# Kernel optimization log

Hardware: AMD Instinct MI355X
Metric: run time of the kernel (lower is better)

Reference implementation:

```python
import jax, jax.numpy as jnp
import numpy as np

# FrictionConfig constants (chosen in init_kwargs)
K_STEPS = 4
ETA = 0.1
ETA_DECAY = 0.9
MU_MAX = 10.0
SMOOTH_LAMBDA = 0.1
RADIUS = 8
B, S, H = 4, 2048, 1024
INNER = max(H // 2, 32)  # 512


def _build_window_edges(length, radius):
    chunks = []
    for d in range(1, radius + 1):
        i = np.arange(length - d, dtype=np.int32)
        chunks.append(np.stack([i, i + d], axis=1))
    return np.concatenate(chunks, axis=0)  # [E, 2]


def setup_inputs() -> dict:
    key = jax.random.key(0)
    ks = jax.random.split(key, 8)
    hidden = jax.random.normal(ks[0], (B, S, H), dtype=jnp.float32)
    attention_mask = jnp.ones((B, S), dtype=jnp.int32)
    edges = jnp.asarray(_build_window_edges(S, RADIUS))
    # edge_mlp: Linear(2, INNER) -> GELU -> Linear(INNER, 1)
    W1 = jax.random.normal(ks[1], (2, INNER), dtype=jnp.float32) * (1.0 / np.sqrt(2))
    b1 = jnp.zeros((INNER,), dtype=jnp.float32)
    W2 = jax.random.normal(ks[2], (INNER, 1), dtype=jnp.float32) * (1.0 / np.sqrt(INNER))
    b2 = jnp.zeros((1,), dtype=jnp.float32)
    # q_proj: Linear(H, H)
    Wq = jax.random.normal(ks[3], (H, H), dtype=jnp.float32) * (1.0 / np.sqrt(H))
    bq = jnp.zeros((H,), dtype=jnp.float32)
    # LayerNorm
    gamma = jnp.ones((H,), dtype=jnp.float32)
    beta = jnp.zeros((H,), dtype=jnp.float32)
    return {"hidden": hidden, "attention_mask": attention_mask, "edges": edges,
            "Wq": Wq, "bq": bq, "W1": W1, "b1": b1, "W2": W2, "b2": b2,
            "gamma": gamma, "beta": beta}


def _edge_weights(h, ei, ej, W1, b1, W2, b2):
    hi = h[ei]  # [E, H]
    hj = h[ej]
    diff = hi - hj
    dist = jnp.linalg.norm(diff, axis=-1, keepdims=True)           # [E, 1]
    ni = jnp.maximum(jnp.linalg.norm(hi, axis=-1), 1e-6)
    nj = jnp.maximum(jnp.linalg.norm(hj, axis=-1), 1e-6)
    cos = (jnp.sum(hi * hj, axis=-1) / (ni * nj))[:, None]         # [E, 1]
    feats = jnp.concatenate([dist, cos], axis=-1)                  # [E, 2]
    z = jax.nn.gelu(feats @ W1 + b1, approximate=False) @ W2 + b2  # [E, 1]
    return jax.nn.softplus(z) + 1e-5


def _laplacian(h, ei, ej, mu):
    n = h.shape[0]
    weighted = mu * (h[ei] - h[ej])  # [E, H]
    # normalize_laplacian = True
    w = mu[:, 0]
    deg = jnp.zeros((n,), h.dtype).at[ei].add(w).at[ej].add(w)
    inv_sqrt = jnp.maximum(deg, 1e-6) ** -0.5
    weighted = weighted * (inv_sqrt[ei] * inv_sqrt[ej])[:, None]
    lap = jnp.zeros_like(h).at[ei].add(weighted).at[ej].add(-weighted)
    return lap


def _smooth(s):
    left = jnp.concatenate([s[:1], s[:-1]], axis=0)
    right = jnp.concatenate([s[1:], s[-1:]], axis=0)
    return s - SMOOTH_LAMBDA * (2.0 * s - left - right)


def _layernorm(x, gamma, beta):
    m = x.mean(axis=-1, keepdims=True)
    v = x.var(axis=-1, keepdims=True)
    return (x - m) * jax.lax.rsqrt(v + 1e-5) * gamma + beta


def _run_single(h, ei, ej, Wq, bq, W1, b1, W2, b2, gamma, beta):
    q = h @ Wq + bq
    state = h
    mu = None
    for step in range(K_STEPS):
        mu = _edge_weights(state, ei, ej, W1, b1, W2, b2)  # recompute_mu=True
        mu = jnp.minimum(mu, MU_MAX)
        lap = _laplacian(state, ei, ej, mu)
        eta = ETA * (ETA_DECAY ** step)
        state = state - eta * (lap - q)
        state = _smooth(state)
    out = _layernorm(state + h, gamma, beta)
    diffs = state[ei] - state[ej]
    energy = 0.5 * jnp.sum(mu[:, 0] * jnp.sum(diffs * diffs, axis=-1))
    return out, energy


def reference(hidden, attention_mask, edges, Wq, bq, W1, b1, W2, b2, gamma, beta):
    # All masks are full-length, so edges are identical across batch and
    # the outer Python batch loop vectorizes to a vmap.
    ei, ej = edges[:, 0], edges[:, 1]
    outputs, energy = jax.vmap(
        lambda h: _run_single(h, ei, ej, Wq, bq, W1, b1, W2, b2, gamma, beta)
    )(hidden)
    return outputs, energy
```

## Files before the change

### kernel.cpp

```cpp
#include <hip/hip_runtime.h>

#define BB 4
#define SS 2048
#define HH 1024
#define TQ 32
#define TU 32
#define CW 256

typedef unsigned short u16;
typedef __bf16 bf16x8 __attribute__((ext_vector_type(8)));
typedef float f32x4 __attribute__((ext_vector_type(4)));

__device__ __forceinline__ float b2f(u16 u){
  union { unsigned int i; float f; } v; v.i = ((unsigned int)u) << 16; return v.f;
}
__device__ __forceinline__ u16 f2b(float f){
  union { float f; unsigned int i; } v; v.f = f;
  unsigned int x = v.i;
  return (u16)((x + 0x7fffu + ((x >> 16) & 1u)) >> 16);
}
__device__ __forceinline__ float4 u4f(ushort4 v){
  float4 o; o.x = b2f(v.x); o.y = b2f(v.y); o.z = b2f(v.z); o.w = b2f(v.w); return o;
}
__device__ __forceinline__ ushort4 f4u(float4 v){
  ushort4 o; o.x = f2b(v.x); o.y = f2b(v.y); o.z = f2b(v.z); o.w = f2b(v.w); return o;
}
__device__ __forceinline__ float wave_sum(float v){
  #pragma unroll
  for(int m = 32; m > 0; m >>= 1) v += __shfl_xor(v, m);
  return v;
}
__device__ __forceinline__ float pread(const void* p, int i, int f){
  return f ? b2f(((const u16*)p)[i]) : ((const float*)p)[i];
}
__device__ __forceinline__ int dflag(const void* gm){
  return (((const u16*)gm)[0] == 0x3F80u) ? 1 : 0;
}
__device__ __forceinline__ void gload16(const void* g, void* l){
  __builtin_amdgcn_global_load_lds((const __attribute__((address_space(1))) unsigned int*)g,
                                   (__attribute__((address_space(3))) unsigned int*)l, 16, 0, 0);
}
__device__ __forceinline__ float  g_load(const float* p){
  return __hip_atomic_load(p, __ATOMIC_RELAXED, __HIP_MEMORY_SCOPE_AGENT);
}
__device__ __forceinline__ float  part_add(float* p, float v){
  return __hip_atomic_fetch_add(p, v, __ATOMIC_RELAXED, __HIP_MEMORY_SCOPE_AGENT);
}
__device__ __forceinline__ int    cnt_add(int* p){
  return __hip_atomic_fetch_add(p, 1, __ATOMIC_RELAXED, __HIP_MEMORY_SCOPE_AGENT);
}

__global__ __launch_bounds__(256) void k_setup(const void* hidden, u16* __restrict__ s,
                                               const void* Wq, u16* __restrict__ Wt,
                                               const void* bq, const void* W1, const void* b1,
                                               const void* W2, const void* b2, const void* gm,
                                               const void* bt,
                                               float* bqc, float* b2c, float* gmc, float* btc,
                                               float4* mlp4s, float* mkeys,
                                               float* partials, int* ecnt){
  __shared__ u16 t[32][33];
  __shared__ float ka[512], kb[512], kc[512], kw[512], kk[512];
  int f = dflag(gm);
  int bid = blockIdx.x, tid = threadIdx.x;
  if(bid < 8192){
    size_t i4 = (size_t)bid*256 + tid;
    if(f){
      ((ushort4*)s)[i4] = ((const ushort4*)hidden)[i4];
    } else {
      ((ushort4*)s)[i4] = f4u(((const float4*)hidden)[i4]);
    }
  } else if(bid < 8192 + 1024){
    int bi = bid - 8192;
    int bx = bi & 31, by = bi >> 5;
    int tx = tid & 31, ty = tid >> 5;
    #pragma unroll
    for(int r = 0; r < 32; r += 8){
      int idx = (by*32 + ty + r)*HH + bx*32 + tx;
      float v = f ? b2f(((const u16*)Wq)[idx]) : ((const float*)Wq)[idx];
      t[ty + r][tx] = f2b(v);
    }
    __syncthreads();
    #pragma unroll
    for(int r = 0; r < 32; r += 8)
      Wt[(size_t)(bx*32 + ty + r)*HH + by*32 + tx] = t[tx][ty + r];
  } else {
    for(int i = tid; i < 1024; i += 256) bqc[i] = pread(bq, i, f);
    if(tid == 0) b2c[0] = pread(b2, 0, f);
    for(int i = tid; i < 1024; i += 256) gmc[i] = pread(gm, i, f);
    for(int i = tid; i < 1024; i += 256) btc[i] = pread(bt, i, f);
    if(tid < BB) partials[tid] = 0.f;
    if(tid == 0) ecnt[0] = 0;
    const float is2 = 0.70710678118654752f;
    for(int j = tid; j < 512; j += 256){
      float a = pread(W1, j, f)       * is2;
      float b = pread(W1, 512 + j, f) * is2;
      float c = pread(b1, j, f)       * is2;
      float w = pread(W2, j, f)       * is2;
      ka[j] = a; kb[j] = b; kc[j] = c; kw[j] = w;
      float aa = fabsf(a);
      kk[j] = (aa > 0.f) ? (4.f + fabsf(b) + fabsf(c)) * __builtin_amdgcn_rcpf(aa) : 3e38f;
    }
    __syncthreads();
    for(int j = tid; j < 512; j += 256){
      float kj = kk[j];
      int r = 0;
      for(int k = 0; k < 512; k++)
        r += (kk[k] < kj) || (kk[k] == kj && k < j);
      mlp4s[r] = make_float4(ka[j], kb[j], kc[j], kw[j]);
      mkeys[r] = kj;
    }
  }
}

__global__ __launch_bounds__(256) void k_qgemm(const u16* __restrict__ A, const u16* __restrict__ Wt,
                                               const float* __restrict__ bqc, u16* __restrict__ q){
  __shared__ u16 lA[128*32];
  __shared__ u16 lB[128*32];
  int m0 = blockIdx.x*128, n0 = blockIdx.y*128;
  int tid  = threadIdx.x;
  int wave = tid >> 6, lane = tid & 63;
  int wm = (wave >> 1)*64, wn = (wave & 1)*64;
  int quad = lane >> 4, l16 = lane & 15;
  int srow = tid >> 2;
  int scol = (tid & 3)*8;

  f32x4 acc[4][4];
  #pragma unroll
  for(int i = 0; i < 4; i++)
    #pragma unroll
    for(int j = 0; j < 4; j++) acc[i][j] = (f32x4){0.f,0.f,0.f,0.f};

  for(int k0 = 0; k0 < HH; k0 += 32){
    __syncthreads();
    gload16(A  + (size_t)(m0 + srow     )*HH + k0 + scol, &lA[ srow     *32 + scol]);
    gload16(A  + (size_t)(m0 + srow + 64)*HH + k0 + scol, &lA[(srow+64) *32 + scol]);
    gload16(Wt + (size_t)(n0 + srow     )*HH + k0 + scol, &lB[ srow     *32 + scol]);
    gload16(Wt + (size_t)(n0 + srow + 64)*HH + k0 + scol, &lB[(srow+64) *32 + scol]);
    __syncthreads();
    bf16x8 af[4];
    #pragma unroll
    for(int mt = 0; mt < 4; mt++)
      af[mt] = *(const bf16x8*)&lA[(wm + mt*16 + l16)*32 + quad*8];
    #pragma unroll
    for(int nt = 0; nt < 4; nt++){
      bf16x8 bf = *(const bf16x8*)&lB[(wn + nt*16 + l16)*32 + quad*8];
      #pragma unroll
      for(int mt = 0; mt < 4; mt++)
        acc[mt][nt] = __builtin_amdgcn_mfma_f32_16x16x32_bf16(af[mt], bf, acc[mt][nt], 0, 0, 0);
    }
  }
  #pragma unroll
  for(int nt = 0; nt < 4; nt++){
    int col = n0 + wn + nt*16 + l16;
    float bqv = bqc[col];
    #pragma unroll
    for(int mt = 0; mt < 4; mt++){
      #pragma unroll
      for(int r = 0; r < 4; r++){
        int row = m0 + wm + mt*16 + quad*4 + r;
        q[(size_t)row*HH + col] = f2b(acc[mt][nt][r] + bqv);
      }
    }
  }
}

__device__ __forceinline__ void gram_band8(const u16* __restrict__ s, int b, int i0,
                                           float* __restrict__ Gband, int tid){
  int wave = tid >> 6, lane = tid & 63;
  if(wave < 4){
    int ti = wave >> 1;
    int tj = (wave + 1) >> 1;
    int quad = lane >> 4, l16 = lane & 15;
    int ra = i0 + ti*16 + l16; if(ra > SS-1) ra = SS-1;
    int rb = i0 + tj*16 + l16; if(rb > SS-1) rb = SS-1;
    const u16* ar = s + ((size_t)b*SS + ra)*HH + quad*8;
    const u16* br = s + ((size_t)b*SS + rb)*HH + quad*8;
    f32x4 acc = (f32x4){0.f,0.f,0.f,0.f};
    #pragma unroll 8
    for(int k0 = 0; k0 < HH; k0 += 32){
      bf16x8 af = *(const bf16x8*)(ar + k0);
      bf16x8 bf = *(const bf16x8*)(br + k0);
      acc = __builtin_amdgcn_mfma_f32_16x16x32_bf16(af, bf, acc, 0, 0, 0);
    }
    #pragma unroll
    for(int r = 0; r < 4; r++){
      int gr = ti*16 + quad*4 + r;
      int dd = tj*16 + l16 - gr;
      if(dd >= 0 && dd <= 8) Gband[gr*9 + dd] = acc[r];
    }
  } else {
    for(int rr = wave - 4; rr < 8; rr += 4){
      int r = 32 + rr;
      int row = i0 + r; if(row > SS-1) row = SS-1;
      const ushort4* rp = (const ushort4*)(s + ((size_t)b*SS + row)*HH);
      float a = 0.f;
      #pragma unroll
      for(int c = 0; c < 4; c++){
        float4 v = u4f(rp[lane + 64*c]);
        a += v.x*v.x + v.y*v.y + v.z*v.z + v.w*v.w;
      }
      a = wave_sum(a);
      if(lane == 0) Gband[r*9] = a;
    }
  }
}

__global__ __launch_bounds__(512) void k_mu(const u16* __restrict__ s,
                                            const float4* __restrict__ mlp4s,
                                            const float* __restrict__ mkeys,
                                            const float* __restrict__ b2c,
                                            float* __restrict__ mu){
  __shared__ float Gband[40*9];
  __shared__ float4 wpk[512];
  __shared__ float skey[512];
  int b = blockIdx.y, i0 = blockIdx.x*TQ;
  int tid = threadIdx.x;
  wpk[tid] = mlp4s[tid]; skey[tid] = mkeys[tid];
  gram_band8(s, b, i0, Gband, tid);
  __syncthreads();

  int e = tid >> 1, h = tid & 1;
  int d = (e >> 5) + 1, k = e & 31;
  bool valid = (i0 + k + d) < SS;
  float gii = Gband[k*9], gjj = Gband[(k+d)*9], gij = Gband[k*9 + d];
  float dist = sqrtf(fmaxf(gii + gjj - 2.f*gij, 0.f));
  float ni = fmaxf(sqrtf(gii), 1e-6f);
  float nj = fmaxf(sqrtf(gjj), 1e-6f);
  float cosv = gij * __builtin_amdgcn_rcpf(ni * nj);
  if(!valid){ dist = 3e38f; cosv = 0.f; }

  float wmin = dist;
  #pragma unroll
  for(int m = 32; m > 0; m >>= 1) wmin = fminf(wmin, __shfl_xor(wmin, m));
  int lo = 0, hi = 512;
  while(lo < hi){ int mid = (lo + hi) >> 1; if(skey[mid] <= wmin) lo = mid + 1; else hi = mid; }
  int cut = lo - h*256; cut = (cut < 0) ? 0 : (cut > 256 ? 256 : cut);

  const float4* wp = &wpk[h*256];
  float acc = 0.f;
  int j = 0;
  #pragma unroll 4
  for(; j < cut; j++){
    float4 wv = wp[j];
    float x = fmaf(dist, wv.x, fmaf(cosv, wv.y, wv.z));
    acc = fmaf(x + fabsf(x), wv.w, acc);
  }
  #pragma unroll 2
  for(; j < 256; j++){
    float4 wv = wp[j];
    float x  = fmaf(dist, wv.x, fmaf(cosv, wv.y, wv.z));
    float ax = fabsf(x);
    float tt = __builtin_amdgcn_rcpf(fmaf(0.3275911f, ax, 1.f));
    float poly = ((((1.061405429f*tt - 1.453152027f)*tt + 1.421413741f)*tt
                   - 0.284496736f)*tt + 0.254829592f)*tt;
    float ape = ax * poly * __expf(-ax*ax);
    acc = fmaf(x + ax - ape, wv.w, acc);
  }
  acc += __shfl_xor(acc, 1);
  if(h == 0 && valid){
    float z  = acc + b2c[0];
    float sp = fmaxf(z, 0.f) + __logf(1.f + __expf(-fabsf(z)));
    mu[((size_t)b*8 + (d-1))*SS + (i0 + k)] = fminf(sp + 1e-5f, 10.0f);
  }
}

__global__ __launch_bounds__(256, 4) void k_upsm(const u16* __restrict__ sIn, u16* __restrict__ sOut,
                                                 const u16* __restrict__ q, const float* __restrict__ mu,
                                                 float eta){
  __shared__ u16 st[50*CW];
  __shared__ float invsS[50];
  __shared__ float muS[58*8];
  int i0 = blockIdx.x*TU, c0 = blockIdx.y*CW, b = blockIdx.z;
  int tid = threadIdx.x;

  for(int idx = tid; idx < 50*(CW/8); idx += 256){
    int r = idx >> 5, cc = idx & 31;
    int i = i0 - 9 + r;
    uint4 v = {0,0,0,0};
    if(i >= 0 && i < SS) v = *(const uint4*)(sIn + ((size_t)b*SS + i)*HH + c0 + cc*8);
    ((uint4*)st)[idx] = v;
  }
  for(int idx = tid; idx < 58*8; idx += 256){
    int ir = idx >> 3, d = (idx & 7) + 1;
    int i = i0 - 17 + ir;
    float v = 0.f;
    if(i >= 0 && i + d < SS) v = mu[((size_t)b*8 + d-1)*SS + i];
    muS[idx] = v;
  }
  __syncthreads();
  if(tid < 50){
    int ir = tid + 8;
    float deg = 0.f;
    #pragma unroll
    for(int d = 1; d <= 8; d++){
      deg += muS[ir*8 + d-1];
      deg += muS[(ir-d)*8 + d-1];
    }
    invsS[tid] = 1.0f / sqrtf(fmaxf(deg, 1e-6f));
  }
  __syncthreads();

  int rq = tid >> 6, lane = tid & 63;
  float4 ua = {0,0,0,0}, ub = {0,0,0,0}, uc = {0,0,0,0};
  #pragma unroll
  for(int k = 0; k < 10; k++){
    int ur = rq*8 + k;
    int i  = i0 - 1 + ur;
    float4 o = {0.f,0.f,0.f,0.f};
    if(i >= 0 && i < SS){
      int sr = ur + 8, vr = ur + 8, mr = ur + 16;
      float inv_i = invsS[vr];
      float4 si = u4f(((const ushort4*)(st + (size_t)sr*CW))[lane]);
      float A = 0.f;
      float4 acc = {0.f,0.f,0.f,0.f};
      #pragma unroll
      for(int d = 1; d <= 8; d++){
        float cR = muS[mr*8 + d-1]     * inv_i        * invsS[vr+d];
        float cL = muS[(mr-d)*8 + d-1] * invsS[vr-d]  * inv_i;
        A += cR + cL;
        float4 vR = u4f(((const ushort4*)(st + (size_t)(sr+d)*CW))[lane]);
        float4 vL = u4f(((const ushort4*)(st + (size_t)(sr-d)*CW))[lane]);
        acc.x -= cR*vR.x + cL*vL.x; acc.y -= cR*vR.y + cL*vL.y;
        acc.z -= cR*vR.z + cL*vL.z; acc.w -= cR*vR.w + cL*vL.w;
      }
      acc.x += A*si.x; acc.y += A*si.y; acc.z += A*si.z; acc.w += A*si.w;
      float4 qv = u4f(*(const ushort4*)(q + ((size_t)b*SS + i)*HH + c0 + lane*4));
      o.x = si.x - eta*(acc.x - qv.x);
      o.y = si.y - eta*(acc.y - qv.y);
      o.z = si.z - eta*(acc.z - qv.z);
      o.w = si.w - eta*(acc.w - qv.w);
    }
    ua = ub; ub = uc; uc = o;
    if(k >= 2){
      int rr = rq*8 + k - 2;
      int iout = i0 + rr;
      float4 cc2 = ub;
      float4 l  = (iout > 0)     ? ua : cc2;
      float4 r4 = (iout < SS-1)  ? uc : cc2;
      float4 oo;
      oo.x = cc2.x - 0.1f*(2.f*cc2.x - l.x - r4.x);
      oo.y = cc2.y - 0.1f*(2.f*cc2.y - l.y - r4.y);
      oo.z = cc2.z - 0.1f*(2.f*cc2.z - l.z - r4.z);
      oo.w = cc2.w - 0.1f*(2.f*cc2.w - l.w - r4.w);
      *(ushort4*)(sOut + ((size_t)b*SS + iout)*HH + c0 + lane*4) = f4u(oo);
    }
  }
}

__global__ __launch_bounds__(256) void k_out(const u16* __restrict__ sA, const void* __restrict__ hraw,
                                             const float* __restrict__ gmc, const float* __restrict__ btc,
                                             void* __restrict__ outp, const void* __restrict__ gmraw){
  int f = dflag(gmraw);
  int b = blockIdx.x >> 11, i = blockIdx.x & (SS-1);
  int tid = threadIdx.x;
  size_t row = (size_t)b*SS + i;
  float4 sv = u4f(((const ushort4*)(sA + row*HH))[tid]);
  float4 hv;
  if(f) hv = u4f(((const ushort4*)((const u16*)hraw + row*HH))[tid]);
  else  hv = ((const float4*)((const float*)hraw + row*HH))[tid];
  float x0 = sv.x + hv.x, x1 = sv.y + hv.y, x2 = sv.z + hv.z, x3 = sv.w + hv.w;

  __shared__ float sh[4];
  int wv = tid >> 6, lane = tid & 63;
  float lsum = wave_sum(x0 + x1 + x2 + x3);
  if(lane == 0) sh[wv] = lsum;
  __syncthreads();
  float mean = (sh[0] + sh[1] + sh[2] + sh[3]) * (1.f/HH);
  __syncthreads();
  float d0 = x0-mean, d1 = x1-mean, d2 = x2-mean, d3 = x3-mean;
  float lsq = wave_sum(d0*d0 + d1*d1 + d2*d2 + d3*d3);
  if(lane == 0) sh[wv] = lsq;
  __syncthreads();
  float var = (sh[0] + sh[1] + sh[2] + sh[3]) * (1.f/HH);
  float sc = 1.0f / sqrtf(var + 1e-5f);

  int col = tid*4;
  float4 o;
  o.x = d0*sc*gmc[col+0] + btc[col+0];
  o.y = d1*sc*gmc[col+1] + btc[col+1];
  o.z = d2*sc*gmc[col+2] + btc[col+2];
  o.w = d3*sc*gmc[col+3] + btc[col+3];
  if(f) ((ushort4*)((u16*)outp + row*HH))[tid] = f4u(o);
  else  ((float4*)((float*)outp + row*HH))[tid] = o;
}

__global__ __launch_bounds__(512) void k_energy(const u16* __restrict__ s, const float* __restrict__ mu,
                                                float* __restrict__ partials, int* __restrict__ ecnt,
                                                void* __restrict__ outp, const void* __restrict__ gmraw){
  __shared__ float Gband[40*9];
  __shared__ float wacc[8];
  int b = blockIdx.y, i0 = blockIdx.x*TQ;
  int tid = threadIdx.x, wave = tid >> 6, lane = tid & 63;
  gram_band8(s, b, i0, Gband, tid);
  __syncthreads();

  int d = wave + 1;
  int k = lane;
  float esum = 0.f;
  if(k < 32 && (i0 + k + d) < SS){
    float d2 = fmaxf(Gband[k*9] + Gband[(k+d)*9] - 2.f*Gband[k*9 + d], 0.f);
    esum = mu[((size_t)b*8 + (d-1))*SS + (i0 + k)] * d2;
  }
  esum = wave_sum(esum);
  if(lane == 0) wacc[wave] = esum;
  __syncthreads();
  if(tid == 0){
    float t = 0.f;
    #pragma unroll
    for(int w2 = 0; w2 < 8; w2++) t += wacc[w2];
    part_add(&partials[b], t);
  }
  __syncthreads();
  if(tid == 0){
    int old = cnt_add(ecnt);
    if(old == (SS/TQ)*BB - 1){
      int f = dflag(gmraw);
      #pragma unroll
      for(int bb = 0; bb < BB; bb++){
        float e = 0.5f * g_load(&partials[bb]);
        if(f) ((u16*)outp)[(size_t)BB*SS*HH + bb] = f2b(e);
        else  ((float*)outp)[(size_t)BB*SS*HH + bb] = e;
      }
    }
  }
}

extern "C" void kernel_launch(void* const* d_in, const int* in_sizes, int n_in,
                              void* d_out, int out_size, void* d_ws, size_t ws_size,
                              hipStream_t stream) {
  const void* hidden = d_in[0];
  const void* Wq  = d_in[3];
  const void* bq  = d_in[4];
  const void* W1  = d_in[5];
  const void* b1  = d_in[6];
  const void* W2  = d_in[7];
  const void* b2v = d_in[8];
  const void* gamma = d_in[9];
  const void* beta  = d_in[10];

  char* w = (char*)d_ws;
  u16*   q   = (u16*)w;     w += (size_t)BB*SS*HH*2;
  u16*   sA  = (u16*)w;     w += (size_t)BB*SS*HH*2;
  u16*   Wt  = (u16*)w;     w += (size_t)HH*HH*2;
  float* mu  = (float*)w;   w += (size_t)BB*8*SS*4;
  float4* mlp4s = (float4*)w; w += 512*16;
  float* mkeys = (float*)w; w += 512*4;
  float* bqc = (float*)w;   w += 1024*4;
  float* b2c = (float*)w;   w += 16;
  float* gmc = (float*)w;   w += 1024*4;
  float* btc = (float*)w;   w += 1024*4;
  float* partials = (float*)w; w += 16;
  int*   ecnt = (int*)w;    w += 16;
  u16* sB = (u16*)d_out;

  k_setup<<<8192 + 1024 + 1, 256, 0, stream>>>(hidden, sA, Wq, Wt, bq, W1, b1, W2, b2v,
                                               gamma, beta, bqc, b2c, gmc, btc,
                                               mlp4s, mkeys, partials, ecnt);
  k_qgemm<<<dim3(BB*SS/128, HH/128), 256, 0, stream>>>(sA, Wt, bqc, q);

  const float etas[4] = {0.1f, 0.09f, 0.081f, 0.0729f};
  for(int step = 0; step < 4; step++){
    const u16* cur = (step & 1) ? sB : sA;
    u16*       nxt = (step & 1) ? sA : sB;
    k_mu  <<<dim3(SS/TQ, BB), 512, 0, stream>>>(cur, mlp4s, mkeys, b2c, mu);
    k_upsm<<<dim3(SS/TU, HH/CW, BB), 256, 0, stream>>>(cur, nxt, q, mu, etas[step]);
  }
  k_out   <<<BB*SS, 256, 0, stream>>>(sA, hidden, gmc, btc, d_out, gamma);
  k_energy<<<dim3(SS/TQ, BB), 512, 0, stream>>>(sA, mu, partials, ecnt, d_out, gamma);
}
```

Baseline: 391.8 us.

## Split gram band into column-partitioned kernel and parallelize edge MLP across more blocks

The fused gram+MLP kernel is split into k_gram, which computes partial banded Gram sums over four 256-column slices in separate blocks, and k_mumlp, which reduces those partials and evaluates the edge MLP. Each MLP block now handles two diagonals with four lanes per edge, giving 1024 blocks instead of 256. The energy kernel reuses the same partial Gram path. The update/smooth kernel tile drops from 32 to 16 rows with a higher occupancy hint. The aim is more parallelism on the latency-bound gram/MLP stage, at the cost of extra launches, a global partial buffer, and more halo reloads in the smaller update tiles.

```diff
diff --git a/kernel.cpp b/kernel.cpp
--- a/kernel.cpp
+++ b/kernel.cpp
@@ -4,7 +4,7 @@
 #define SS 2048
 #define HH 1024
 #define TQ 32
-#define TU 32
+#define TU 16
 #define CW 256
 
 typedef unsigned short u16;
@@ -164,65 +164,73 @@
   }
 }
 
-__device__ __forceinline__ void gram_band8(const u16* __restrict__ s, int b, int i0,
-                                           float* __restrict__ Gband, int tid){
-  int wave = tid >> 6, lane = tid & 63;
-  if(wave < 4){
-    int ti = wave >> 1;
-    int tj = (wave + 1) >> 1;
-    int quad = lane >> 4, l16 = lane & 15;
-    int ra = i0 + ti*16 + l16; if(ra > SS-1) ra = SS-1;
-    int rb = i0 + tj*16 + l16; if(rb > SS-1) rb = SS-1;
-    const u16* ar = s + ((size_t)b*SS + ra)*HH + quad*8;
-    const u16* br = s + ((size_t)b*SS + rb)*HH + quad*8;
-    f32x4 acc = (f32x4){0.f,0.f,0.f,0.f};
-    #pragma unroll 8
-    for(int k0 = 0; k0 < HH; k0 += 32){
-      bf16x8 af = *(const bf16x8*)(ar + k0);
-      bf16x8 bf = *(const bf16x8*)(br + k0);
-      acc = __builtin_amdgcn_mfma_f32_16x16x32_bf16(af, bf, acc, 0, 0, 0);
-    }
-    #pragma unroll
-    for(int r = 0; r < 4; r++){
-      int gr = ti*16 + quad*4 + r;
-      int dd = tj*16 + l16 - gr;
-      if(dd >= 0 && dd <= 8) Gband[gr*9 + dd] = acc[r];
-    }
-  } else {
-    for(int rr = wave - 4; rr < 8; rr += 4){
-      int r = 32 + rr;
-      int row = i0 + r; if(row > SS-1) row = SS-1;
-      const ushort4* rp = (const ushort4*)(s + ((size_t)b*SS + row)*HH);
-      float a = 0.f;
-      #pragma unroll
-      for(int c = 0; c < 4; c++){
-        float4 v = u4f(rp[lane + 64*c]);
-        a += v.x*v.x + v.y*v.y + v.z*v.z + v.w*v.w;
-      }
-      a = wave_sum(a);
-      if(lane == 0) Gband[r*9] = a;
-    }
-  }
-}
-
-__global__ __launch_bounds__(512) void k_mu(const u16* __restrict__ s,
-                                            const float4* __restrict__ mlp4s,
-                                            const float* __restrict__ mkeys,
-                                            const float* __restrict__ b2c,
-                                            float* __restrict__ mu){
-  __shared__ float Gband[40*9];
+__global__ __launch_bounds__(256) void k_gram(const u16* __restrict__ s, float* __restrict__ Gpart){
+  int tile = blockIdx.x, sub = blockIdx.y, b = blockIdx.z;
+  int i0 = tile*TQ, cb = sub*256;
+  int tid = threadIdx.x, wave = tid >> 6, lane = tid & 63;
+  float* gp = Gpart + (((size_t)b*64 + tile)*4 + sub)*360;
+
+  int ti = wave >> 1;
+  int tj = (wave + 1) >> 1;
+  int quad = lane >> 4, l16 = lane & 15;
+  int ra = i0 + ti*16 + l16; if(ra > SS-1) ra = SS-1;
+  int rb = i0 + tj*16 + l16; if(rb > SS-1) rb = SS-1;
+  const u16* ar = s + ((size_t)b*SS + ra)*HH + cb + quad*8;
+  const u16* br = s + ((size_t)b*SS + rb)*HH + cb + quad*8;
+  f32x4 acc = (f32x4){0.f,0.f,0.f,0.f};
+  #pragma unroll
+  for(int k0 = 0; k0 < 256; k0 += 32){
+    bf16x8 af = *(const bf16x8*)(ar + k0);
+    bf16x8 bf = *(const bf16x8*)(br + k0);
+    acc = __builtin_amdgcn_mfma_f32_16x16x32_bf16(af, bf, acc, 0, 0, 0);
+  }
+  #pragma unroll
+  for(int r = 0; r < 4; r++){
+    int gr = ti*16 + quad*4 + r;
+    int dd = tj*16 + l16 - gr;
+    if(dd >= 0 && dd <= 8) gp[gr*9 + dd] = acc[r];
+  }
+  #pragma unroll
+  for(int jj = 0; jj < 2; jj++){
+    int r = 32 + wave + jj*4;
+    int row = i0 + r; if(row > SS-1) row = SS-1;
+    float4 v = u4f(((const ushort4*)(s + ((size_t)b*SS + row)*HH + cb))[lane]);
+    float a = v.x*v.x + v.y*v.y + v.z*v.z + v.w*v.w;
+    a = wave_sum(a);
+    if(lane == 0) gp[r*9] = a;
+  }
+}
+
+__global__ __launch_bounds__(256) void k_mumlp(const float* __restrict__ Gpart,
+                                               const float4* __restrict__ mlp4s,
+                                               const float* __restrict__ mkeys,
+                                               const float* __restrict__ b2c,
+                                               float* __restrict__ mu){
+  __shared__ float Gd[40];
+  __shared__ float Gq[2][32];
   __shared__ float4 wpk[512];
   __shared__ float skey[512];
-  int b = blockIdx.y, i0 = blockIdx.x*TQ;
+  int tile = blockIdx.x, sub = blockIdx.y, b = blockIdx.z;
+  int i0 = tile*TQ;
   int tid = threadIdx.x;
-  wpk[tid] = mlp4s[tid]; skey[tid] = mkeys[tid];
-  gram_band8(s, b, i0, Gband, tid);
-  __syncthreads();
-
-  int e = tid >> 1, h = tid & 1;
-  int d = (e >> 5) + 1, k = e & 31;
+  const float* g0 = Gpart + ((size_t)b*64 + tile)*4*360;
+
+  if(tid < 40)
+    Gd[tid] = (g0[tid*9] + g0[360 + tid*9]) + (g0[720 + tid*9] + g0[1080 + tid*9]);
+  else if(tid >= 64 && tid < 128){
+    int idx = tid - 64, k = idx & 31, dl = idx >> 5;
+    int d = sub*2 + dl + 1;
+    Gq[dl][k] = (g0[k*9 + d] + g0[360 + k*9 + d]) + (g0[720 + k*9 + d] + g0[1080 + k*9 + d]);
+  }
+  #pragma unroll
+  for(int j = 0; j < 2; j++){ wpk[tid + 256*j] = mlp4s[tid + 256*j]; skey[tid + 256*j] = mkeys[tid + 256*j]; }
+  __syncthreads();
+
+  int el = tid >> 2, qd = tid & 3;
+  int dl = el >> 5, k = el & 31;
+  int d = sub*2 + dl + 1;
   bool valid = (i0 + k + d) < SS;
-  float gii = Gband[k*9], gjj = Gband[(k+d)*9], gij = Gband[k*9 + d];
+  float gii = Gd[k], gjj = Gd[k + d], gij = Gq[dl][k];
   float dist = sqrtf(fmaxf(gii + gjj - 2.f*gij, 0.f));
   float ni = fmaxf(sqrtf(gii), 1e-6f);
   float nj = fmaxf(sqrtf(gjj), 1e-6f);
@@ -234,20 +242,19 @@
   for(int m = 32; m > 0; m >>= 1) wmin = fminf(wmin, __shfl_xor(wmin, m));
   int lo = 0, hi = 512;
   while(lo < hi){ int mid = (lo + hi) >> 1; if(skey[mid] <= wmin) lo = mid + 1; else hi = mid; }
-  int cut = lo - h*256; cut = (cut < 0) ? 0 : (cut > 256 ? 256 : cut);
-
-  const float4* wp = &wpk[h*256];
+  int j0cut = lo >> 2;
+
   float acc = 0.f;
-  int j = 0;
+  int j0 = 0;
   #pragma unroll 4
-  for(; j < cut; j++){
-    float4 wv = wp[j];
+  for(; j0 < j0cut; j0++){
+    float4 wv = wpk[qd + 4*j0];
     float x = fmaf(dist, wv.x, fmaf(cosv, wv.y, wv.z));
     acc = fmaf(x + fabsf(x), wv.w, acc);
   }
   #pragma unroll 2
-  for(; j < 256; j++){
-    float4 wv = wp[j];
+  for(; j0 < 128; j0++){
+    float4 wv = wpk[qd + 4*j0];
     float x  = fmaf(dist, wv.x, fmaf(cosv, wv.y, wv.z));
     float ax = fabsf(x);
     float tt = __builtin_amdgcn_rcpf(fmaf(0.3275911f, ax, 1.f));
@@ -257,30 +264,31 @@
     acc = fmaf(x + ax - ape, wv.w, acc);
   }
   acc += __shfl_xor(acc, 1);
-  if(h == 0 && valid){
+  acc += __shfl_xor(acc, 2);
+  if(qd == 0 && valid){
     float z  = acc + b2c[0];
     float sp = fmaxf(z, 0.f) + __logf(1.f + __expf(-fabsf(z)));
     mu[((size_t)b*8 + (d-1))*SS + (i0 + k)] = fminf(sp + 1e-5f, 10.0f);
   }
 }
 
-__global__ __launch_bounds__(256, 4) void k_upsm(const u16* __restrict__ sIn, u16* __restrict__ sOut,
+__global__ __launch_bounds__(256, 8) void k_upsm(const u16* __restrict__ sIn, u16* __restrict__ sOut,
                                                  const u16* __restrict__ q, const float* __restrict__ mu,
                                                  float eta){
-  __shared__ u16 st[50*CW];
-  __shared__ float invsS[50];
-  __shared__ float muS[58*8];
+  __shared__ u16 st[34*CW];
+  __shared__ float invsS[34];
+  __shared__ float muS[42*8];
   int i0 = blockIdx.x*TU, c0 = blockIdx.y*CW, b = blockIdx.z;
   int tid = threadIdx.x;
 
-  for(int idx = tid; idx < 50*(CW/8); idx += 256){
+  for(int idx = tid; idx < 34*(CW/8); idx += 256){
     int r = idx >> 5, cc = idx & 31;
     int i = i0 - 9 + r;
     uint4 v = {0,0,0,0};
     if(i >= 0 && i < SS) v = *(const uint4*)(sIn + ((size_t)b*SS + i)*HH + c0 + cc*8);
     ((uint4*)st)[idx] = v;
   }
-  for(int idx = tid; idx < 58*8; idx += 256){
+  for(int idx = tid; idx < 42*8; idx += 256){
     int ir = idx >> 3, d = (idx & 7) + 1;
     int i = i0 - 17 + ir;
     float v = 0.f;
@@ -288,7 +296,7 @@
     muS[idx] = v;
   }
   __syncthreads();
-  if(tid < 50){
+  if(tid < 34){
     int ir = tid + 8;
     float deg = 0.f;
     #pragma unroll
@@ -303,8 +311,8 @@
   int rq = tid >> 6, lane = tid & 63;
   float4 ua = {0,0,0,0}, ub = {0,0,0,0}, uc = {0,0,0,0};
   #pragma unroll
-  for(int k = 0; k < 10; k++){
-    int ur = rq*8 + k;
+  for(int k = 0; k < 6; k++){
+    int ur = rq*4 + k;
     int i  = i0 - 1 + ur;
     float4 o = {0.f,0.f,0.f,0.f};
     if(i >= 0 && i < SS){
@@ -332,7 +340,7 @@
     }
     ua = ub; ub = uc; uc = o;
     if(k >= 2){
-      int rr = rq*8 + k - 2;
+      int rr = rq*4 + k - 2;
       int iout = i0 + rr;
       float4 cc2 = ub;
       float4 l  = (iout > 0)     ? ua : cc2;
@@ -384,36 +392,40 @@
   else  ((float4*)((float*)outp + row*HH))[tid] = o;
 }
 
-__global__ __launch_bounds__(512) void k_energy(const u16* __restrict__ s, const float* __restrict__ mu,
-                                                float* __restrict__ partials, int* __restrict__ ecnt,
-                                                void* __restrict__ outp, const void* __restrict__ gmraw){
-  __shared__ float Gband[40*9];
-  __shared__ float wacc[8];
-  int b = blockIdx.y, i0 = blockIdx.x*TQ;
+__global__ __launch_bounds__(256) void k_efin(const float* __restrict__ Gpart, const float* __restrict__ mu,
+                                              float* __restrict__ partials, int* __restrict__ ecnt,
+                                              void* __restrict__ outp, const void* __restrict__ gmraw){
+  __shared__ float Gd[40];
+  __shared__ float Gq[8][32];
+  __shared__ float wacc[4];
+  int tile = blockIdx.x, b = blockIdx.y;
+  int i0 = tile*TQ;
   int tid = threadIdx.x, wave = tid >> 6, lane = tid & 63;
-  gram_band8(s, b, i0, Gband, tid);
-  __syncthreads();
-
-  int d = wave + 1;
-  int k = lane;
+  const float* g0 = Gpart + ((size_t)b*64 + tile)*4*360;
+
+  if(tid < 40)
+    Gd[tid] = (g0[tid*9] + g0[360 + tid*9]) + (g0[720 + tid*9] + g0[1080 + tid*9]);
+  {
+    int k = tid & 31, dl = tid >> 5, d = dl + 1;
+    Gq[dl][k] = (g0[k*9 + d] + g0[360 + k*9 + d]) + (g0[720 + k*9 + d] + g0[1080 + k*9 + d]);
+  }
+  __syncthreads();
+
+  int k = tid & 31, d = (tid >> 5) + 1;
   float esum = 0.f;
-  if(k < 32 && (i0 + k + d) < SS){
-    float d2 = fmaxf(Gband[k*9] + Gband[(k+d)*9] - 2.f*Gband[k*9 + d], 0.f);
+  if((i0 + k + d) < SS){
+    float d2 = fmaxf(Gd[k] + Gd[k + d] - 2.f*Gq[d-1][k], 0.f);
     esum = mu[((size_t)b*8 + (d-1))*SS + (i0 + k)] * d2;
   }
   esum = wave_sum(esum);
   if(lane == 0) wacc[wave] = esum;
   __syncthreads();
-  if(tid == 0){
-    float t = 0.f;
-    #pragma unroll
-    for(int w2 = 0; w2 < 8; w2++) t += wacc[w2];
-    part_add(&partials[b], t);
-  }
+  if(tid == 0)
+    part_add(&partials[b], (wacc[0] + wacc[1]) + (wacc[2] + wacc[3]));
   __syncthreads();
   if(tid == 0){
     int old = cnt_add(ecnt);
-    if(old == (SS/TQ)*BB - 1){
+    if(old == 64*BB - 1){
       int f = dflag(gmraw);
       #pragma unroll
       for(int bb = 0; bb < BB; bb++){
@@ -443,6 +455,7 @@
   u16*   sA  = (u16*)w;     w += (size_t)BB*SS*HH*2;
   u16*   Wt  = (u16*)w;     w += (size_t)HH*HH*2;
   float* mu  = (float*)w;   w += (size_t)BB*8*SS*4;
+  float* Gpart = (float*)w; w += (size_t)BB*64*4*360*4;
   float4* mlp4s = (float4*)w; w += 512*16;
   float* mkeys = (float*)w; w += 512*4;
   float* bqc = (float*)w;   w += 1024*4;
@@ -462,9 +475,11 @@
   for(int step = 0; step < 4; step++){
     const u16* cur = (step & 1) ? sB : sA;
     u16*       nxt = (step & 1) ? sA : sB;
-    k_mu  <<<dim3(SS/TQ, BB), 512, 0, stream>>>(cur, mlp4s, mkeys, b2c, mu);
-    k_upsm<<<dim3(SS/TU, HH/CW, BB), 256, 0, stream>>>(cur, nxt, q, mu, etas[step]);
-  }
-  k_out   <<<BB*SS, 256, 0, stream>>>(sA, hidden, gmc, btc, d_out, gamma);
-  k_energy<<<dim3(SS/TQ, BB), 512, 0, stream>>>(sA, mu, partials, ecnt, d_out, gamma);
-}
+    k_gram <<<dim3(64, 4, BB), 256, 0, stream>>>(cur, Gpart);
+    k_mumlp<<<dim3(64, 4, BB), 256, 0, stream>>>(Gpart, mlp4s, mkeys, b2c, mu);
+    k_upsm <<<dim3(SS/TU, HH/CW, BB), 256, 0, stream>>>(cur, nxt, q, mu, etas[step]);
+  }
+  k_out <<<BB*SS, 256, 0, stream>>>(sA, hidden, gmc, btc, d_out, gamma);
+  k_gram<<<dim3(64, 4, BB), 256, 0, stream>>>(sA, Gpart);
+  k_efin<<<dim3(64, BB), 256, 0, stream>>>(Gpart, mu, partials, ecnt, d_out, gamma);
+}
```

New measurement: 524.0 us. 1.34x slower.
